# Optimization experiments

Measured on AMD Instinct MI355X. Metric: run time of the kernel, lower is better.

Reference implementation:

```python
import jax, jax.numpy as jnp
import numpy as np

SCALE = 1.0 / np.sqrt(128.0)  # 1/sqrt(head_size)
NEG = -1000000000.0


def setup_inputs() -> dict:
    key = jax.random.key(0)
    k1, k2, k3, k4 = jax.random.split(key, 4)
    B, H, S, D = 2, 16, 2048, 128
    q = jax.random.normal(k1, (B, H, S, D), dtype=jnp.float32)
    k = jax.random.normal(k2, (B, H, S, D), dtype=jnp.float32)
    v = jax.random.normal(k3, (B, H, S, D), dtype=jnp.float32)
    mask = jax.random.randint(k4, (B, S), 0, 2, dtype=jnp.int32)
    return {"q": q, "k": k, "v": v, "mask": mask}


def reference(q, k, v, mask):
    # scores: [B, H, Sq, Sk]
    scores = jnp.einsum("bhqd,bhkd->bhqk", q, k) * SCALE
    m = mask[:, None, None, :]  # [B,1,1,Sk], broadcast over heads and queries
    scores = jnp.where(m == 0, NEG, scores)
    weights = jax.nn.softmax(scores, axis=-1)
    out = jnp.einsum("bhqk,bhkd->bhqd", weights, v)
    return out
```

## Files before the change

### kernel.cpp

```cpp
#include <hip/hip_runtime.h>
#include <hip/hip_bf16.h>

typedef __attribute__((ext_vector_type(8))) short short8;
typedef __attribute__((ext_vector_type(4))) short short4_;
typedef __attribute__((ext_vector_type(4))) float floatx4;

#define NB 2
#define NH 16
#define NBH 32
#define SS 2048
#define DD 128
#define BQ 128
#define BK 32
#define SCALE 0.08838834764831845f
#define LOG2E 1.4426950408889634f
#define MAXB 12.0f
#define KTILES (SS / BK)

__device__ __forceinline__ short f2bf(float f) {
  union { float f; unsigned u; } x; x.f = f;
  return (short)((x.u + 0x7FFFu + ((x.u >> 16) & 1u)) >> 16);
}

__device__ __forceinline__ void gload_lds16(const short* g, short* l) {
  __builtin_amdgcn_global_load_lds(
      (const __attribute__((address_space(1))) void*)(g),
      (__attribute__((address_space(3))) void*)(l), 16, 0, 0);
}

__global__ __launch_bounds__(256) void cvt_kernel(const float* __restrict__ in,
                                                  short* __restrict__ out) {
  int i = blockIdx.x * 256 + threadIdx.x;
  const float4* p = (const float4*)(in + (size_t)i * 8);
  float4 a = p[0], b = p[1];
  short8 o;
  o[0] = f2bf(a.x); o[1] = f2bf(a.y); o[2] = f2bf(a.z); o[3] = f2bf(a.w);
  o[4] = f2bf(b.x); o[5] = f2bf(b.y); o[6] = f2bf(b.z); o[7] = f2bf(b.w);
  *(short8*)(out + (size_t)i * 8) = o;
}

__global__ __launch_bounds__(256) void vT_kernel(const float* __restrict__ v,
                                                 short* __restrict__ vtg) {
  __shared__ short Ts[32][36];
  int kt = blockIdx.x, dt = blockIdx.y, bh = blockIdx.z;
  int tid = threadIdx.x;
  int row = tid >> 3, cs = tid & 7;
  const float* src = v + ((size_t)bh * SS + kt * 32 + row) * DD + dt * 32 + cs * 4;
  float4 x = *(const float4*)src;
  short4_ s;
  s[0] = f2bf(x.x); s[1] = f2bf(x.y); s[2] = f2bf(x.z); s[3] = f2bf(x.w);
  *(short4_*)&Ts[row][cs * 4] = s;
  __syncthreads();
  short4_ o;
#pragma unroll
  for (int i = 0; i < 4; ++i) o[i] = Ts[cs * 4 + i][row];
  *(short4_*)(vtg + ((size_t)bh * DD + dt * 32 + row) * SS + kt * 32 + cs * 4) = o;
}

__global__ __launch_bounds__(256, 2) void fa_kernel(
    const float* __restrict__ q, const short* __restrict__ kbf,
    const short* __restrict__ vtg, const int* __restrict__ mask,
    float* __restrict__ out) {
  __shared__ short Ks[BK * DD];
  __shared__ short Vt[DD * BK];
  __shared__ short Ps[4][2][16 * 32];

  const int tid = threadIdx.x;
  const int wave = tid >> 6;
  const int lane = tid & 63;
  const int l16 = lane & 15;
  const int quad = lane >> 4;
  const int bh = blockIdx.y;
  const int b = bh >> 4;
  const int q0 = blockIdx.x * BQ;

  const size_t base = (size_t)bh * SS * DD;
  const float* qg = q + base;
  const short* kg = kbf + base;
  const short* vg = vtg + base;
  const int* mg = mask + b * SS;
  const float c1 = SCALE * LOG2E, c2 = MAXB * LOG2E;

  short8 qf[2][4];
#pragma unroll
  for (int t = 0; t < 2; ++t) {
    int qrow = q0 + wave * 32 + t * 16 + l16;
    const float* qp = qg + (size_t)qrow * DD;
#pragma unroll
    for (int dc = 0; dc < 4; ++dc) {
      const float* p = qp + dc * 32 + quad * 8;
      float4 a = *(const float4*)p;
      float4 bb = *(const float4*)(p + 4);
      short8 tt;
      tt[0] = f2bf(a.x); tt[1] = f2bf(a.y); tt[2] = f2bf(a.z); tt[3] = f2bf(a.w);
      tt[4] = f2bf(bb.x); tt[5] = f2bf(bb.y); tt[6] = f2bf(bb.z); tt[7] = f2bf(bb.w);
      qf[t][dc] = tt;
    }
  }

  floatx4 Oacc[2][8];
#pragma unroll
  for (int t = 0; t < 2; ++t)
#pragma unroll
    for (int f = 0; f < 8; ++f) Oacc[t][f] = (floatx4){0.f, 0.f, 0.f, 0.f};
  float l_acc[2][4];
#pragma unroll
  for (int t = 0; t < 2; ++t)
#pragma unroll
    for (int r = 0; r < 4; ++r) l_acc[t][r] = 0.f;

  for (int kt = 0; kt < KTILES; ++kt) {
    __syncthreads();
#pragma unroll
    for (int i = 0; i < 2; ++i) {
      int c = wave + i * 4;
      {
        int row = c * 4 + (lane >> 4);
        int slot = lane & 15;
        const short* src = kg + ((size_t)(kt * BK + row)) * DD + ((slot ^ (row & 7)) * 8);
        gload_lds16(src, Ks + c * 512);
      }
      {
        int d = c * 16 + (lane >> 2);
        int slot = lane & 3;
        const short* src = vg + (size_t)d * SS + kt * BK + ((slot ^ (d & 3)) * 8);
        gload_lds16(src, Vt + c * 512);
      }
    }
    __syncthreads();

    floatx4 sacc[2][2];
#pragma unroll
    for (int t = 0; t < 2; ++t)
#pragma unroll
      for (int nt = 0; nt < 2; ++nt) sacc[t][nt] = (floatx4){0.f, 0.f, 0.f, 0.f};
#pragma unroll
    for (int nt = 0; nt < 2; ++nt) {
      int row = nt * 16 + l16;
#pragma unroll
      for (int dc = 0; dc < 4; ++dc) {
        int g = dc * 4 + quad;
        short8 kf = *(const short8*)(Ks + row * DD + ((g ^ (row & 7)) * 8));
        sacc[0][nt] = __builtin_amdgcn_mfma_f32_16x16x32_bf16(qf[0][dc], kf, sacc[0][nt], 0, 0, 0);
        sacc[1][nt] = __builtin_amdgcn_mfma_f32_16x16x32_bf16(qf[1][dc], kf, sacc[1][nt], 0, 0, 0);
      }
    }

    int mv0 = mg[kt * BK + l16];
    int mv1 = mg[kt * BK + 16 + l16];
    short8 pf[2];
#pragma unroll
    for (int t = 0; t < 2; ++t) {
      float p0[4], p1[4];
#pragma unroll
      for (int r = 0; r < 4; ++r) {
        float e0 = exp2f(fmaf(sacc[t][0][r], c1, -c2));
        float e1 = exp2f(fmaf(sacc[t][1][r], c1, -c2));
        p0[r] = mv0 ? e0 : 0.f;
        p1[r] = mv1 ? e1 : 0.f;
        l_acc[t][r] += p0[r] + p1[r];
      }
      short* pp = &Ps[wave][t][0];
#pragma unroll
      for (int r = 0; r < 4; ++r) {
        int row = quad * 4 + r;
        int g0 = l16 >> 3, g1 = 2 + (l16 >> 3);
        pp[row * 32 + ((g0 ^ quad) * 8) + (l16 & 7)] = f2bf(p0[r]);
        pp[row * 32 + ((g1 ^ quad) * 8) + (l16 & 7)] = f2bf(p1[r]);
      }
      pf[t] = *(const short8*)(pp + l16 * 32 + ((quad ^ (l16 >> 2)) * 8));
    }

#pragma unroll
    for (int f = 0; f < 8; ++f) {
      int d = f * 16 + l16;
      short8 vf = *(const short8*)(Vt + d * 32 + ((quad ^ (d & 3)) * 8));
      Oacc[0][f] = __builtin_amdgcn_mfma_f32_16x16x32_bf16(pf[0], vf, Oacc[0][f], 0, 0, 0);
      Oacc[1][f] = __builtin_amdgcn_mfma_f32_16x16x32_bf16(pf[1], vf, Oacc[1][f], 0, 0, 0);
    }
  }

  float* og = out + base;
#pragma unroll
  for (int t = 0; t < 2; ++t) {
    float inv[4];
#pragma unroll
    for (int r = 0; r < 4; ++r) {
      float s = l_acc[t][r];
#pragma unroll
      for (int off = 8; off >= 1; off >>= 1) s += __shfl_xor(s, off, 16);
      inv[r] = 1.0f / s;
    }
#pragma unroll
    for (int r = 0; r < 4; ++r) {
      int row = q0 + wave * 32 + t * 16 + quad * 4 + r;
      float* orow = og + (size_t)row * DD;
#pragma unroll
      for (int f = 0; f < 8; ++f)
        orow[f * 16 + l16] = Oacc[t][f][r] * inv[r];
    }
  }
}

extern "C" void kernel_launch(void* const* d_in, const int* in_sizes, int n_in,
                              void* d_out, int out_size, void* d_ws, size_t ws_size,
                              hipStream_t stream) {
  const float* q = (const float*)d_in[0];
  const float* k = (const float*)d_in[1];
  const float* v = (const float*)d_in[2];
  const int* mask = (const int*)d_in[3];
  float* out = (float*)d_out;

  short* kbf = (short*)d_ws;
  short* vtg = kbf + (size_t)NBH * SS * DD;

  cvt_kernel<<<dim3((NBH * SS * DD) / (256 * 8)), dim3(256), 0, stream>>>(k, kbf);
  vT_kernel<<<dim3(SS / 32, DD / 32, NBH), dim3(256), 0, stream>>>(v, vtg);
  fa_kernel<<<dim3(SS / BQ, NBH), dim3(256), 0, stream>>>(q, kbf, vtg, mask, out);
}
```

Measured before the change: 244.1 us.

## Transpose score MFMA to keep P in registers and merge K/V prep kernels

Swaps the MFMA operand order so the score tile comes out transposed, which lets each lane feed its exponentiated probabilities straight into 16x16x16 bf16 MFMAs for the PV product. This removes the per-tile LDS round-trip for P. K conversion and V transpose are merged into one prep kernel, and mask reads become int4 vector loads. Addresses are precomputed outside the loop, and output stores become float4. The costs are twice as many smaller MFMAs for PV, plus a cheaper bf16 rounding that does not handle NaN or ties exactly.

```diff
diff --git a/kernel.cpp b/kernel.cpp
--- a/kernel.cpp
+++ b/kernel.cpp
@@ -2,7 +2,7 @@
 #include <hip/hip_bf16.h>
 
 typedef __attribute__((ext_vector_type(8))) short short8;
-typedef __attribute__((ext_vector_type(4))) short short4_;
+typedef __attribute__((ext_vector_type(4))) short short4v;
 typedef __attribute__((ext_vector_type(4))) float floatx4;
 
 #define NB 2
@@ -12,14 +12,30 @@
 #define DD 128
 #define BQ 128
 #define BK 32
+#define KTILES (SS / BK)
 #define SCALE 0.08838834764831845f
 #define LOG2E 1.4426950408889634f
 #define MAXB 12.0f
-#define KTILES (SS / BK)
+
+#if __has_builtin(__builtin_amdgcn_mfma_f32_16x16x16bf16_1k)
+#define MFMA16(a, b, c) __builtin_amdgcn_mfma_f32_16x16x16bf16_1k(a, b, c, 0, 0, 0)
+#elif __has_builtin(__builtin_amdgcn_mfma_f32_16x16x16_bf16)
+#define MFMA16(a, b, c) __builtin_amdgcn_mfma_f32_16x16x16_bf16(a, b, c, 0, 0, 0)
+#else
+__device__ __forceinline__ floatx4 mfma16_asm(short4v a, short4v b, floatx4 c) {
+  asm volatile("v_mfma_f32_16x16x16_bf16 %0, %1, %2, %0" : "+v"(c) : "v"(a), "v"(b));
+  return c;
+}
+#define MFMA16(a, b, c) mfma16_asm(a, b, c)
+#endif
 
 __device__ __forceinline__ short f2bf(float f) {
   union { float f; unsigned u; } x; x.f = f;
   return (short)((x.u + 0x7FFFu + ((x.u >> 16) & 1u)) >> 16);
+}
+__device__ __forceinline__ short f2bf_fast(float f) {
+  union { float f; unsigned u; } x; x.f = f;
+  return (short)((x.u + 0x8000u) >> 16);
 }
 
 __device__ __forceinline__ void gload_lds16(const short* g, short* l) {
@@ -28,42 +44,51 @@
       (__attribute__((address_space(3))) void*)(l), 16, 0, 0);
 }
 
-__global__ __launch_bounds__(256) void cvt_kernel(const float* __restrict__ in,
-                                                  short* __restrict__ out) {
-  int i = blockIdx.x * 256 + threadIdx.x;
-  const float4* p = (const float4*)(in + (size_t)i * 8);
-  float4 a = p[0], b = p[1];
-  short8 o;
-  o[0] = f2bf(a.x); o[1] = f2bf(a.y); o[2] = f2bf(a.z); o[3] = f2bf(a.w);
-  o[4] = f2bf(b.x); o[5] = f2bf(b.y); o[6] = f2bf(b.z); o[7] = f2bf(b.w);
-  *(short8*)(out + (size_t)i * 8) = o;
-}
-
-__global__ __launch_bounds__(256) void vT_kernel(const float* __restrict__ v,
-                                                 short* __restrict__ vtg) {
-  __shared__ short Ts[32][36];
-  int kt = blockIdx.x, dt = blockIdx.y, bh = blockIdx.z;
-  int tid = threadIdx.x;
-  int row = tid >> 3, cs = tid & 7;
-  const float* src = v + ((size_t)bh * SS + kt * 32 + row) * DD + dt * 32 + cs * 4;
-  float4 x = *(const float4*)src;
-  short4_ s;
-  s[0] = f2bf(x.x); s[1] = f2bf(x.y); s[2] = f2bf(x.z); s[3] = f2bf(x.w);
-  *(short4_*)&Ts[row][cs * 4] = s;
+__global__ __launch_bounds__(256) void prep_kernel(const float* __restrict__ k,
+                                                   const float* __restrict__ v,
+                                                   short* __restrict__ kbf,
+                                                   short* __restrict__ vtg) {
+  __shared__ short Ts[DD][68];
+  const int kb = blockIdx.x, bh = blockIdx.y;
+  const int tid = threadIdx.x;
+  const size_t base = (size_t)bh * SS * DD + (size_t)(kb * 64) * DD;
+  const float* kr = k + base;
+  const float* vr = v + base;
+  short* kw = kbf + base;
+#pragma unroll
+  for (int c = 0; c < 8; ++c) {
+    int fi = c * 256 + tid;
+    float4 a = ((const float4*)kr)[fi];
+    short4v o;
+    o[0] = f2bf(a.x); o[1] = f2bf(a.y); o[2] = f2bf(a.z); o[3] = f2bf(a.w);
+    *(short4v*)(kw + (size_t)fi * 4) = o;
+    float4 vv = ((const float4*)vr)[fi];
+    int d0 = (fi * 4) & 127, key = (fi * 4) >> 7;
+    Ts[d0 + 0][key] = f2bf(vv.x);
+    Ts[d0 + 1][key] = f2bf(vv.y);
+    Ts[d0 + 2][key] = f2bf(vv.z);
+    Ts[d0 + 3][key] = f2bf(vv.w);
+  }
   __syncthreads();
-  short4_ o;
-#pragma unroll
-  for (int i = 0; i < 4; ++i) o[i] = Ts[cs * 4 + i][row];
-  *(short4_*)(vtg + ((size_t)bh * DD + dt * 32 + row) * SS + kt * 32 + cs * 4) = o;
+#pragma unroll
+  for (int s = 0; s < 4; ++s) {
+    int d = s * 32 + (tid >> 3);
+    int c = tid & 7, kt2 = c >> 2, g = c & 3;
+    short4v lo = *(short4v*)&Ts[d][kt2 * 32 + g * 4];
+    short4v hi = *(short4v*)&Ts[d][kt2 * 32 + 16 + g * 4];
+    short8 o;
+#pragma unroll
+    for (int r = 0; r < 4; ++r) { o[r] = lo[r]; o[4 + r] = hi[r]; }
+    *(short8*)(vtg + ((size_t)(bh * DD + d)) * SS + (kb * 2 + kt2) * 32 + g * 8) = o;
+  }
 }
 
 __global__ __launch_bounds__(256, 2) void fa_kernel(
     const float* __restrict__ q, const short* __restrict__ kbf,
     const short* __restrict__ vtg, const int* __restrict__ mask,
     float* __restrict__ out) {
-  __shared__ short Ks[BK * DD];
-  __shared__ short Vt[DD * BK];
-  __shared__ short Ps[4][2][16 * 32];
+  __shared__ __align__(16) short Ks[BK * DD];
+  __shared__ __align__(16) short Vt[DD * BK];
 
   const int tid = threadIdx.x;
   const int wave = tid >> 6;
@@ -77,20 +102,17 @@
   const size_t base = (size_t)bh * SS * DD;
   const float* qg = q + base;
   const short* kg = kbf + base;
-  const short* vg = vtg + base;
-  const int* mg = mask + b * SS;
+  const int4* mg4 = (const int4*)(mask + b * SS);
   const float c1 = SCALE * LOG2E, c2 = MAXB * LOG2E;
 
   short8 qf[2][4];
 #pragma unroll
   for (int t = 0; t < 2; ++t) {
-    int qrow = q0 + wave * 32 + t * 16 + l16;
-    const float* qp = qg + (size_t)qrow * DD;
+    const float* qp = qg + (size_t)(q0 + wave * 32 + t * 16 + l16) * DD;
 #pragma unroll
     for (int dc = 0; dc < 4; ++dc) {
-      const float* p = qp + dc * 32 + quad * 8;
-      float4 a = *(const float4*)p;
-      float4 bb = *(const float4*)(p + 4);
+      float4 a = *(const float4*)(qp + dc * 32 + quad * 8);
+      float4 bb = *(const float4*)(qp + dc * 32 + quad * 8 + 4);
       short8 tt;
       tt[0] = f2bf(a.x); tt[1] = f2bf(a.y); tt[2] = f2bf(a.z); tt[3] = f2bf(a.w);
       tt[4] = f2bf(bb.x); tt[5] = f2bf(bb.y); tt[6] = f2bf(bb.z); tt[7] = f2bf(bb.w);
@@ -103,101 +125,94 @@
   for (int t = 0; t < 2; ++t)
 #pragma unroll
     for (int f = 0; f < 8; ++f) Oacc[t][f] = (floatx4){0.f, 0.f, 0.f, 0.f};
-  float l_acc[2][4];
-#pragma unroll
-  for (int t = 0; t < 2; ++t)
-#pragma unroll
-    for (int r = 0; r < 4; ++r) l_acc[t][r] = 0.f;
+  float l_acc[2] = {0.f, 0.f};
+
+  const short* ksrc[2]; short* kdst[2];
+  const short* vsrc[2]; short* vdst[2];
+#pragma unroll
+  for (int i = 0; i < 2; ++i) {
+    int c = wave * 2 + i;
+    int krow = c * 4 + (lane >> 4), kslot = lane & 15;
+    ksrc[i] = kg + (size_t)krow * DD + ((kslot ^ (krow & 7)) * 8);
+    kdst[i] = Ks + c * 512;
+    int d = c * 16 + (lane >> 2);
+    int g = (lane & 3) ^ ((lane >> 3) & 3);
+    vsrc[i] = vtg + ((size_t)(bh * DD + d)) * SS + g * 8;
+    vdst[i] = Vt + c * 512;
+  }
+  int koff[2];
+#pragma unroll
+  for (int nt = 0; nt < 2; ++nt) koff[nt] = (nt * 16 + l16) * DD;
+  const int ksw = l16 & 7;
+  const int voff = l16 * 32 + ((quad ^ ((l16 >> 1) & 3)) * 8);
 
   for (int kt = 0; kt < KTILES; ++kt) {
     __syncthreads();
 #pragma unroll
     for (int i = 0; i < 2; ++i) {
-      int c = wave + i * 4;
-      {
-        int row = c * 4 + (lane >> 4);
-        int slot = lane & 15;
-        const short* src = kg + ((size_t)(kt * BK + row)) * DD + ((slot ^ (row & 7)) * 8);
-        gload_lds16(src, Ks + c * 512);
+      gload_lds16(ksrc[i] + (size_t)kt * (BK * DD), kdst[i]);
+      gload_lds16(vsrc[i] + kt * BK, vdst[i]);
+    }
+    __syncthreads();
+
+    floatx4 sacc[2][2];
+#pragma unroll
+    for (int t = 0; t < 2; ++t)
+#pragma unroll
+      for (int nt = 0; nt < 2; ++nt) sacc[t][nt] = (floatx4){0.f, 0.f, 0.f, 0.f};
+#pragma unroll
+    for (int nt = 0; nt < 2; ++nt)
+#pragma unroll
+      for (int dc = 0; dc < 4; ++dc) {
+        short8 kf = *(const short8*)(Ks + koff[nt] + (((dc * 4 + quad) ^ ksw) * 8));
+        sacc[0][nt] = __builtin_amdgcn_mfma_f32_16x16x32_bf16(kf, qf[0][dc], sacc[0][nt], 0, 0, 0);
+        sacc[1][nt] = __builtin_amdgcn_mfma_f32_16x16x32_bf16(kf, qf[1][dc], sacc[1][nt], 0, 0, 0);
       }
-      {
-        int d = c * 16 + (lane >> 2);
-        int slot = lane & 3;
-        const short* src = vg + (size_t)d * SS + kt * BK + ((slot ^ (d & 3)) * 8);
-        gload_lds16(src, Vt + c * 512);
-      }
-    }
-    __syncthreads();
-
-    floatx4 sacc[2][2];
-#pragma unroll
-    for (int t = 0; t < 2; ++t)
-#pragma unroll
-      for (int nt = 0; nt < 2; ++nt) sacc[t][nt] = (floatx4){0.f, 0.f, 0.f, 0.f};
-#pragma unroll
-    for (int nt = 0; nt < 2; ++nt) {
-      int row = nt * 16 + l16;
-#pragma unroll
-      for (int dc = 0; dc < 4; ++dc) {
-        int g = dc * 4 + quad;
-        short8 kf = *(const short8*)(Ks + row * DD + ((g ^ (row & 7)) * 8));
-        sacc[0][nt] = __builtin_amdgcn_mfma_f32_16x16x32_bf16(qf[0][dc], kf, sacc[0][nt], 0, 0, 0);
-        sacc[1][nt] = __builtin_amdgcn_mfma_f32_16x16x32_bf16(qf[1][dc], kf, sacc[1][nt], 0, 0, 0);
-      }
-    }
-
-    int mv0 = mg[kt * BK + l16];
-    int mv1 = mg[kt * BK + 16 + l16];
-    short8 pf[2];
+
+    int4 mm0 = mg4[kt * 8 + quad];
+    int4 mm1 = mg4[kt * 8 + 4 + quad];
+    short4v pb[2][2];
 #pragma unroll
     for (int t = 0; t < 2; ++t) {
-      float p0[4], p1[4];
-#pragma unroll
-      for (int r = 0; r < 4; ++r) {
-        float e0 = exp2f(fmaf(sacc[t][0][r], c1, -c2));
-        float e1 = exp2f(fmaf(sacc[t][1][r], c1, -c2));
-        p0[r] = mv0 ? e0 : 0.f;
-        p1[r] = mv1 ? e1 : 0.f;
-        l_acc[t][r] += p0[r] + p1[r];
-      }
-      short* pp = &Ps[wave][t][0];
-#pragma unroll
-      for (int r = 0; r < 4; ++r) {
-        int row = quad * 4 + r;
-        int g0 = l16 >> 3, g1 = 2 + (l16 >> 3);
-        pp[row * 32 + ((g0 ^ quad) * 8) + (l16 & 7)] = f2bf(p0[r]);
-        pp[row * 32 + ((g1 ^ quad) * 8) + (l16 & 7)] = f2bf(p1[r]);
-      }
-      pf[t] = *(const short8*)(pp + l16 * 32 + ((quad ^ (l16 >> 2)) * 8));
+      float p;
+      p = mm0.x ? __builtin_amdgcn_exp2f(fmaf(sacc[t][0][0], c1, -c2)) : 0.f; l_acc[t] += p; pb[t][0][0] = f2bf_fast(p);
+      p = mm0.y ? __builtin_amdgcn_exp2f(fmaf(sacc[t][0][1], c1, -c2)) : 0.f; l_acc[t] += p; pb[t][0][1] = f2bf_fast(p);
+      p = mm0.z ? __builtin_amdgcn_exp2f(fmaf(sacc[t][0][2], c1, -c2)) : 0.f; l_acc[t] += p; pb[t][0][2] = f2bf_fast(p);
+      p = mm0.w ? __builtin_amdgcn_exp2f(fmaf(sacc[t][0][3], c1, -c2)) : 0.f; l_acc[t] += p; pb[t][0][3] = f2bf_fast(p);
+      p = mm1.x ? __builtin_amdgcn_exp2f(fmaf(sacc[t][1][0], c1, -c2)) : 0.f; l_acc[t] += p; pb[t][1][0] = f2bf_fast(p);
+      p = mm1.y ? __builtin_amdgcn_exp2f(fmaf(sacc[t][1][1], c1, -c2)) : 0.f; l_acc[t] += p; pb[t][1][1] = f2bf_fast(p);
+      p = mm1.z ? __builtin_amdgcn_exp2f(fmaf(sacc[t][1][2], c1, -c2)) : 0.f; l_acc[t] += p; pb[t][1][2] = f2bf_fast(p);
+      p = mm1.w ? __builtin_amdgcn_exp2f(fmaf(sacc[t][1][3], c1, -c2)) : 0.f; l_acc[t] += p; pb[t][1][3] = f2bf_fast(p);
     }
 
 #pragma unroll
     for (int f = 0; f < 8; ++f) {
-      int d = f * 16 + l16;
-      short8 vf = *(const short8*)(Vt + d * 32 + ((quad ^ (d & 3)) * 8));
-      Oacc[0][f] = __builtin_amdgcn_mfma_f32_16x16x32_bf16(pf[0], vf, Oacc[0][f], 0, 0, 0);
-      Oacc[1][f] = __builtin_amdgcn_mfma_f32_16x16x32_bf16(pf[1], vf, Oacc[1][f], 0, 0, 0);
+      short8 vv = *(const short8*)(Vt + f * 512 + voff);
+      short4v va0 = __builtin_shufflevector(vv, vv, 0, 1, 2, 3);
+      short4v va1 = __builtin_shufflevector(vv, vv, 4, 5, 6, 7);
+      Oacc[0][f] = MFMA16(va0, pb[0][0], Oacc[0][f]);
+      Oacc[0][f] = MFMA16(va1, pb[0][1], Oacc[0][f]);
+      Oacc[1][f] = MFMA16(va0, pb[1][0], Oacc[1][f]);
+      Oacc[1][f] = MFMA16(va1, pb[1][1], Oacc[1][f]);
     }
   }
 
   float* og = out + base;
 #pragma unroll
   for (int t = 0; t < 2; ++t) {
-    float inv[4];
-#pragma unroll
-    for (int r = 0; r < 4; ++r) {
-      float s = l_acc[t][r];
-#pragma unroll
-      for (int off = 8; off >= 1; off >>= 1) s += __shfl_xor(s, off, 16);
-      inv[r] = 1.0f / s;
-    }
-#pragma unroll
-    for (int r = 0; r < 4; ++r) {
-      int row = q0 + wave * 32 + t * 16 + quad * 4 + r;
-      float* orow = og + (size_t)row * DD;
-#pragma unroll
-      for (int f = 0; f < 8; ++f)
-        orow[f * 16 + l16] = Oacc[t][f][r] * inv[r];
+    float s = l_acc[t];
+    s += __shfl_xor(s, 16);
+    s += __shfl_xor(s, 32);
+    float inv = 1.0f / s;
+    float* orow = og + (size_t)(q0 + wave * 32 + t * 16 + l16) * DD + quad * 4;
+#pragma unroll
+    for (int f = 0; f < 8; ++f) {
+      float4 w;
+      w.x = Oacc[t][f][0] * inv;
+      w.y = Oacc[t][f][1] * inv;
+      w.z = Oacc[t][f][2] * inv;
+      w.w = Oacc[t][f][3] * inv;
+      *(float4*)(orow + f * 16) = w;
     }
   }
 }
@@ -214,7 +229,6 @@
   short* kbf = (short*)d_ws;
   short* vtg = kbf + (size_t)NBH * SS * DD;
 
-  cvt_kernel<<<dim3((NBH * SS * DD) / (256 * 8)), dim3(256), 0, stream>>>(k, kbf);
-  vT_kernel<<<dim3(SS / 32, DD / 32, NBH), dim3(256), 0, stream>>>(v, vtg);
+  prep_kernel<<<dim3(SS / 64, NBH), dim3(256), 0, stream>>>(k, v, kbf, vtg);
   fa_kernel<<<dim3(SS / BQ, NBH), dim3(256), 0, stream>>>(q, kbf, vtg, mask, out);
 }
```

Result: faster. 237.7 us (-2.6%).
